# Kernel optimization log

Hardware: AMD Instinct MI355X
Metric: run time of the kernel (lower is better)

Reference implementation:

```python
import jax, jax.numpy as jnp
import numpy as np

N = 100000
E = 3200000
FIRE, WEA, TER = 8, 12, 10
H = 64


def setup_inputs() -> dict:
    key = jax.random.key(0)
    ks = jax.random.split(key, 24)
    def lin(kw, fan_in, fan_out):
        # torch nn.Linear default init: U(-1/sqrt(fan_in), 1/sqrt(fan_in))
        b = 1.0 / np.sqrt(fan_in)
        W = jax.random.uniform(kw, (fan_in, fan_out), jnp.float32, -b, b)
        return W
    inp = {
        'x_fire': jax.random.normal(ks[0], (N, FIRE), jnp.float32),
        'x_weather': jax.random.normal(ks[1], (N, WEA), jnp.float32),
        'x_terrain': jax.random.normal(ks[2], (N, TER), jnp.float32),
        'edge_index': jax.random.randint(ks[3], (2, E), 0, N, jnp.int64),
        # modality encoders
        'w_fire': lin(ks[4], FIRE, H), 'b_fire': jnp.zeros((H,), jnp.float32),
        'w_wea': lin(ks[5], WEA, H),  'b_wea': jnp.zeros((H,), jnp.float32),
        'w_ter': lin(ks[6], TER, H),  'b_ter': jnp.zeros((H,), jnp.float32),
        # GCN layers (concat fusion -> first layer in_dim = 3H)
        'gcn_w0': lin(ks[7], 3 * H, H), 'gcn_b0': jnp.zeros((H,), jnp.float32),
        'gcn_w1': lin(ks[8], H, H),     'gcn_b1': jnp.zeros((H,), jnp.float32),
        'gcn_w2': lin(ks[9], H, H),     'gcn_b2': jnp.zeros((H,), jnp.float32),
        # output MLP: H -> H//2 -> 1
        'out_w1': lin(ks[10], H, H // 2), 'out_b1': jnp.zeros((H // 2,), jnp.float32),
        'out_w2': lin(ks[11], H // 2, 1), 'out_b2': jnp.zeros((1,), jnp.float32),
    }
    return inp


def _gcn_conv(x, src, dst, W, b):
    """PyG GCNConv: h = W x; out[i] = sum_{j->i} norm_ij h[j] + self-loop + bias,
    with norm_ij = deg[i]^-1/2 * deg[j]^-1/2, deg including the added self-loop."""
    h = x @ W                                             # [N, H]
    deg = jnp.zeros((N,), h.dtype).at[dst].add(1.0) + 1.0  # +1 self-loop
    dinv = jax.lax.rsqrt(deg)                             # deg^-0.5
    norm = dinv[src] * dinv[dst]                          # [E]
    agg = jnp.zeros_like(h).at[dst].add(h[src] * norm[:, None])
    agg = agg + h * (dinv * dinv)[:, None]                # self-loop contribution
    return agg + b


def reference(x_fire, x_weather, x_terrain, edge_index,
              w_fire, b_fire, w_wea, b_wea, w_ter, b_ter,
              gcn_w0, gcn_b0, gcn_w1, gcn_b1, gcn_w2, gcn_b2,
              out_w1, out_b1, out_w2, out_b2):
    # modality encoders (eval mode: dropout is identity)
    h_fire = jax.nn.relu(x_fire @ w_fire + b_fire)
    h_wea = jax.nn.relu(x_weather @ w_wea + b_wea)
    h_ter = jax.nn.relu(x_terrain @ w_ter + b_ter)
    x = jnp.concatenate([h_fire, h_wea, h_ter], axis=1)   # [N, 3H]
    src, dst = edge_index[0], edge_index[1]
    x = jax.nn.relu(_gcn_conv(x, src, dst, gcn_w0, gcn_b0))
    x = jax.nn.relu(_gcn_conv(x, src, dst, gcn_w1, gcn_b1))
    x = jax.nn.relu(_gcn_conv(x, src, dst, gcn_w2, gcn_b2))
    out = jax.nn.relu(x @ out_w1 + out_b1) @ out_w2 + out_b2
    return out
```

## Files before the change

kernel.cpp:

```cpp
#include <hip/hip_runtime.h>

#define NN 100000
#define NE 3200000
#define HD 64

#define NBUCK 256
#define BWID 392
#define SLACK 20480
#define COLCAP 13568
#define OVFCAP 512
#define CAP 16
#define P1_EPB 2048
#define P1_GRID ((NE + P1_EPB - 1) / P1_EPB)

typedef int      v4i __attribute__((ext_vector_type(4)));
typedef int      v2i __attribute__((ext_vector_type(2)));
typedef _Float16 h4f __attribute__((ext_vector_type(4)));

__device__ __forceinline__ void fma4(float4& a, float s, const float4& b) {
    a.x = fmaf(s, b.x, a.x); a.y = fmaf(s, b.y, a.y);
    a.z = fmaf(s, b.z, a.z); a.w = fmaf(s, b.w, a.w);
}
__device__ __forceinline__ void addh4(float4& a, const h4f& b) {
    a.x += (float)b[0]; a.y += (float)b[1]; a.z += (float)b[2]; a.w += (float)b[3];
}

__global__ void __launch_bounds__(256) partition_kernel(
    const int* __restrict__ src, const int* __restrict__ dst,
    int* __restrict__ bctl, v2i* __restrict__ pairs, v2i* __restrict__ povf) {
    __shared__ v2i stage[NBUCK][CAP];
    __shared__ int cnt[NBUCK];
    int t = threadIdx.x;
    cnt[t] = 0;
    __syncthreads();
    const v4i* d4p = (const v4i*)dst;
    const v4i* s4p = (const v4i*)src;
    const int NE4 = NE / 4;
    int base4 = blockIdx.x * (P1_EPB / 4);
    #pragma unroll
    for (int it = 0; it < P1_EPB / 1024; it++) {
        int i = base4 + it * 256 + t;
        v4i d4 = (v4i){-1, -1, -1, -1};
        v4i s4 = (v4i){0, 0, 0, 0};
        if (i < NE4) {
            d4 = __builtin_nontemporal_load(d4p + i);
            s4 = __builtin_nontemporal_load(s4p + i);
        }
        #pragma unroll
        for (int k = 0; k < 4; k++) {
            int d = d4[k];
            if (d >= 0) {
                int b = (unsigned)d / BWID;
                int slot = atomicAdd(&cnt[b], 1);
                v2i p; p[0] = s4[k]; p[1] = d;
                if (slot < CAP) {
                    stage[b][slot] = p;
                } else {
                    int o = atomicAdd(&bctl[b * 16 + 2], 1);
                    if (o < OVFCAP) povf[(size_t)b * OVFCAP + o] = p;
                }
            }
        }
    }
    __syncthreads();
    int c_tot = cnt[t];
    int c = (c_tot > CAP) ? CAP : c_tot;
    int runs = (c + 7) >> 3;
    if (runs) {
        int slots = runs * 8;
        for (int m = c; m < slots; m++) { v2i p; p[0] = 0; p[1] = -1; stage[t][m] = p; }
        int gb = atomicAdd(&bctl[t * 16], slots);
        if (gb + slots <= SLACK) {
            v4i* gp = (v4i*)(pairs + (size_t)t * SLACK + gb);
            const v4i* sp = (const v4i*)&stage[t][0];
            #pragma unroll
            for (int m = 0; m < 8; m++) { if (m < runs * 4) gp[m] = sp[m]; }
        } else {
            for (int m = 0; m < slots && gb + m < SLACK; m++)
                pairs[(size_t)t * SLACK + gb + m] = stage[t][m];
        }
    }
    if (c_tot > 0) atomicAdd(&bctl[t * 16 + 1], c_tot);
}

__global__ void bucket_scan_kernel(const int* __restrict__ bctl,
                                   int* __restrict__ bbase, int* __restrict__ rowptr) {
    __shared__ int s[NBUCK];
    int t = threadIdx.x;
    int v = bctl[t * 16 + 1];
    s[t] = v; __syncthreads();
    for (int off = 1; off < NBUCK; off <<= 1) {
        int x = (t >= off) ? s[t - off] : 0;
        __syncthreads();
        s[t] += x;
        __syncthreads();
    }
    bbase[t] = s[t] - v;
    if (t == NBUCK - 1) rowptr[NN] = s[t];
}

__global__ void __launch_bounds__(256) csr_fill_kernel(
    const v2i* __restrict__ pairs, const v2i* __restrict__ povf,
    const int* __restrict__ bctl, const int* __restrict__ bbase,
    int* __restrict__ rowptr, float* __restrict__ dinv, int* __restrict__ col) {
    __shared__ int hist[BWID];
    __shared__ int rp[BWID];
    __shared__ int cur[BWID];
    __shared__ int sc[256];
    __shared__ int cols[COLCAP];
    int b = blockIdx.x, t = threadIdx.x;
    int lo = b * BWID;
    int hi = min(lo + BWID, NN);
    int nw = hi - lo;
    for (int i = t; i < BWID; i += 256) { hist[i] = 0; cur[i] = 0; }
    __syncthreads();
    int np = bctl[b * 16];     if (np > SLACK) np = SLACK;
    int nov = bctl[b * 16 + 2]; if (nov > OVFCAP) nov = OVFCAP;
    int base = bbase[b];
    const v2i* pb = pairs + (size_t)b * SLACK;
    const v2i* ob = povf + (size_t)b * OVFCAP;
    for (int i = t; i < np; i += 256) {
        v2i p = pb[i];
        if (p[1] >= 0) atomicAdd(&hist[p[1] - lo], 1);
    }
    for (int i = t; i < nov; i += 256) {
        v2i p = ob[i];
        atomicAdd(&hist[p[1] - lo], 1);
    }
    __syncthreads();
    int h0 = 0, s2 = 0;
    if (2 * t < BWID) {
        h0 = hist[2 * t];
        int h1 = (2 * t + 1 < BWID) ? hist[2 * t + 1] : 0;
        s2 = h0 + h1;
    }
    sc[t] = s2; __syncthreads();
    for (int off = 1; off < 256; off <<= 1) {
        int x = (t >= off) ? sc[t - off] : 0;
        __syncthreads();
        sc[t] += x;
        __syncthreads();
    }
    if (2 * t < BWID) {
        int ex = sc[t] - s2;
        rp[2 * t] = ex;
        if (2 * t + 1 < BWID) rp[2 * t + 1] = ex + h0;
    }
    __syncthreads();
    for (int i = t; i < nw; i += 256) {
        rowptr[lo + i] = base + rp[i];
        dinv[lo + i] = 1.0f / sqrtf((float)(hist[i] + 1));
    }
    for (int i = t; i < np; i += 256) {
        v2i p = pb[i];
        if (p[1] >= 0) {
            int li = p[1] - lo;
            int slot = atomicAdd(&cur[li], 1);
            int o = rp[li] + slot;
            if (o < COLCAP) cols[o] = p[0];
        }
    }
    for (int i = t; i < nov; i += 256) {
        v2i p = ob[i];
        int li = p[1] - lo;
        int slot = atomicAdd(&cur[li], 1);
        int o = rp[li] + slot;
        if (o < COLCAP) cols[o] = p[0];
    }
    __syncthreads();
    int nreal = bctl[b * 16 + 1]; if (nreal > COLCAP) nreal = COLCAP;
    for (int i = t; i < nreal; i += 256)
        col[base + i] = cols[i];
}

__global__ void __launch_bounds__(256) encmm0_kernel(
    const float* __restrict__ xf, const float* __restrict__ xw, const float* __restrict__ xt,
    const float* __restrict__ Wf, const float* __restrict__ bf,
    const float* __restrict__ Ww, const float* __restrict__ bw,
    const float* __restrict__ Wt, const float* __restrict__ bt,
    const float* __restrict__ W0, const float* __restrict__ dinv,
    _Float16* __restrict__ h) {
    __shared__ float xin[64][32];
    __shared__ float wenc[30][64];
    __shared__ float bs[192];
    __shared__ float xs[64][36];
    __shared__ float ws[32][64];
    int t = threadIdx.x;
    int n0 = blockIdx.x * 64;

    {
        const float4* xf4 = (const float4*)xf;
        for (int i = t; i < 128; i += 256) {
            int n = i >> 1, q = i & 1;
            int gn = n0 + n;
            float4 v = make_float4(0, 0, 0, 0);
            if (gn < NN) v = xf4[(size_t)gn * 2 + q];
            *(float4*)&xin[n][q * 4] = v;
        }
        const float4* xw4 = (const float4*)xw;
        for (int i = t; i < 192; i += 256) {
            int n = i / 3, q = i - n * 3;
            int gn = n0 + n;
            float4 v = make_float4(0, 0, 0, 0);
            if (gn < NN) v = xw4[(size_t)gn * 3 + q];
            *(float4*)&xin[n][8 + q * 4] = v;
        }
        const float2* xt2 = (const float2*)xt;
        for (int i = t; i < 320; i += 256) {
            int n = i / 5, q = i - n * 5;
            int gn = n0 + n;
            float2 v = make_float2(0, 0);
            if (gn < NN) v = xt2[(size_t)gn * 5 + q];
            *(float2*)&xin[n][20 + q * 2] = v;
        }
        for (int i = t; i < 480; i += 256) {
            int r = i >> 4, q = i & 15;
            float4 v;
            if (r < 8)       v = ((const float4*)Wf)[r * 16 + q];
            else if (r < 20) v = ((const float4*)Ww)[(r - 8) * 16 + q];
            else             v = ((const float4*)Wt)[(r - 20) * 16 + q];
            *(float4*)&wenc[r][q * 4] = v;
        }
        if (t < 192) bs[t] = (t < 64) ? bf[t] : (t < 128) ? bw[t - 64] : bt[t - 128];
    }

    int cg = t & 15, ng = t >> 4;
    int c0 = cg * 4;
    float4 acc[4];
    #pragma unroll
    for (int i = 0; i < 4; i++) acc[i] = make_float4(0, 0, 0, 0);

    for (int kq = 0; kq < 6; kq++) {
        __syncthreads();
        {
            const float4* W04 = (const float4*)W0;
            float4* ws4 = (float4*)&ws[0][0];
            for (int i = t; i < 512; i += 256)
                ws4[i] = W04[(size_t)kq * 512 + i];
        }
        int coff = (kq < 2) ? kq * 32 : (kq < 4) ? (kq - 2) * 32 : (kq - 4) * 32;
        if (kq < 2) {
            for (int i = t; i < 2048; i += 256) {
                int n = i >> 5, kk = i & 31;
                float a = bs[kq * 32 + kk];
                #pragma unroll
                for (int k = 0; k < 8; k++) a = fmaf(xin[n][k], wenc[k][coff + kk], a);
                xs[n][kk] = fmaxf(a, 0.f);
            }
        } else if (kq < 4) {
            for (int i = t; i < 2048; i += 256) {
                int n = i >> 5, kk = i & 31;
                float a = bs[kq * 32 + kk];
                #pragma unroll
                for (int k = 0; k < 12; k++) a = fmaf(xin[n][8 + k], wenc[8 + k][coff + kk], a);
                xs[n][kk] = fmaxf(a, 0.f);
            }
        } else {
            for (int i = t; i < 2048; i += 256) {
                int n = i >> 5, kk = i & 31;
                float a = bs[kq * 32 + kk];
                #pragma unroll
                for (int k = 0; k < 10; k++) a = fmaf(xin[n][20 + k], wenc[20 + k][coff + kk], a);
                xs[n][kk] = fmaxf(a, 0.f);
            }
        }
        __syncthreads();
        for (int k = 0; k < 32; k += 4) {
            float4 b0 = *(const float4*)&ws[k + 0][c0];
            float4 b1 = *(const float4*)&ws[k + 1][c0];
            float4 b2 = *(const float4*)&ws[k + 2][c0];
            float4 b3 = *(const float4*)&ws[k + 3][c0];
            #pragma unroll
            for (int i = 0; i < 4; i++) {
                float4 a = *(const float4*)&xs[ng * 4 + i][k];
                fma4(acc[i], a.x, b0); fma4(acc[i], a.y, b1);
                fma4(acc[i], a.z, b2); fma4(acc[i], a.w, b3);
            }
        }
    }
    h4f* h4 = (h4f*)h;
    #pragma unroll
    for (int i = 0; i < 4; i++) {
        int gn = n0 + ng * 4 + i;
        if (gn < NN) {
            float dn = dinv[gn];
            h4f v;
            v[0] = (_Float16)(acc[i].x * dn);
            v[1] = (_Float16)(acc[i].y * dn);
            v[2] = (_Float16)(acc[i].z * dn);
            v[3] = (_Float16)(acc[i].w * dn);
            h4[((unsigned)gn << 4) + cg] = v;
        }
    }
}

#define GATHER_BODY(E)                                              \
    {   int s_ = __shfl(pv, (E));                                   \
        h4f v_ = h4[((unsigned)s_ << 4) + q];                       \
        addh4(acc, v_); }

__global__ void gather_mm_kernel(
    const int* __restrict__ col, const int* __restrict__ rowptr,
    const float* __restrict__ dinv, const _Float16* __restrict__ h,
    const float* __restrict__ bias, const float* __restrict__ W,
    _Float16* __restrict__ hout) {
    int t = threadIdx.x;
    int n = (blockIdx.x * 256 + t) >> 6;
    int l = t & 63;
    if (n >= NN) return;
    int g = l >> 4;
    int q = l & 15;
    const h4f* h4 = (const h4f*)h;
    float dn = dinv[n];
    h4f hnh = h4[((unsigned)n << 4) + q];
    float4 b4 = ((const float4*)bias)[q];
    float4 acc = make_float4(0, 0, 0, 0);
    int r0 = rowptr[n], r1 = rowptr[n + 1];
    for (int base = r0; base < r1; base += 64) {
        int cnt = min(64, r1 - base);
        int pv = NN;
        if (l < cnt) pv = __builtin_nontemporal_load(col + base + l);
        int steps = (cnt + 3) >> 2;
        int j = 0;
        for (; j + 8 <= steps; j += 8) {
            int s0 = __shfl(pv, (j + 0) * 4 + g);
            int s1 = __shfl(pv, (j + 1) * 4 + g);
            int s2 = __shfl(pv, (j + 2) * 4 + g);
            int s3 = __shfl(pv, (j + 3) * 4 + g);
            int s4 = __shfl(pv, (j + 4) * 4 + g);
            int s5 = __shfl(pv, (j + 5) * 4 + g);
            int s6 = __shfl(pv, (j + 6) * 4 + g);
            int s7 = __shfl(pv, (j + 7) * 4 + g);
            h4f v0 = h4[((unsigned)s0 << 4) + q];
            h4f v1 = h4[((unsigned)s1 << 4) + q];
            h4f v2 = h4[((unsigned)s2 << 4) + q];
            h4f v3 = h4[((unsigned)s3 << 4) + q];
            h4f v4 = h4[((unsigned)s4 << 4) + q];
            h4f v5 = h4[((unsigned)s5 << 4) + q];
            h4f v6 = h4[((unsigned)s6 << 4) + q];
            h4f v7 = h4[((unsigned)s7 << 4) + q];
            addh4(acc, v0); addh4(acc, v1); addh4(acc, v2); addh4(acc, v3);
            addh4(acc, v4); addh4(acc, v5); addh4(acc, v6); addh4(acc, v7);
        }
        for (; j + 4 <= steps; j += 4) {
            int s0 = __shfl(pv, (j + 0) * 4 + g);
            int s1 = __shfl(pv, (j + 1) * 4 + g);
            int s2 = __shfl(pv, (j + 2) * 4 + g);
            int s3 = __shfl(pv, (j + 3) * 4 + g);
            h4f v0 = h4[((unsigned)s0 << 4) + q];
            h4f v1 = h4[((unsigned)s1 << 4) + q];
            h4f v2 = h4[((unsigned)s2 << 4) + q];
            h4f v3 = h4[((unsigned)s3 << 4) + q];
            addh4(acc, v0); addh4(acc, v1); addh4(acc, v2); addh4(acc, v3);
        }
        for (; j < steps; j++)
            GATHER_BODY(j * 4 + g)
    }
    acc.x += __shfl_xor(acc.x, 16); acc.y += __shfl_xor(acc.y, 16);
    acc.z += __shfl_xor(acc.z, 16); acc.w += __shfl_xor(acc.w, 16);
    acc.x += __shfl_xor(acc.x, 32); acc.y += __shfl_xor(acc.y, 32);
    acc.z += __shfl_xor(acc.z, 32); acc.w += __shfl_xor(acc.w, 32);
    float4 r;
    r.x = fmaxf(fmaf(dn, acc.x + (float)hnh[0], b4.x), 0.f);
    r.y = fmaxf(fmaf(dn, acc.y + (float)hnh[1], b4.y), 0.f);
    r.z = fmaxf(fmaf(dn, acc.z + (float)hnh[2], b4.z), 0.f);
    r.w = fmaxf(fmaf(dn, acc.w + (float)hnh[3], b4.w), 0.f);
    float oc0 = 0.f, oc1 = 0.f, oc2 = 0.f, oc3 = 0.f;
    #pragma unroll
    for (int qq = 0; qq < 16; qq++) {
        float rx = __shfl(r.x, qq);
        float ry = __shfl(r.y, qq);
        float rz = __shfl(r.z, qq);
        float rw = __shfl(r.w, qq);
        oc0 = fmaf(rx, W[(qq * 4 + 0) * 64 + l], oc0);
        oc1 = fmaf(ry, W[(qq * 4 + 1) * 64 + l], oc1);
        oc2 = fmaf(rz, W[(qq * 4 + 2) * 64 + l], oc2);
        oc3 = fmaf(rw, W[(qq * 4 + 3) * 64 + l], oc3);
    }
    float oc = (oc0 + oc1) + (oc2 + oc3);
    __builtin_nontemporal_store((_Float16)(oc * dn), &hout[((unsigned)n << 6) + l]);
}

__global__ void gather_mlp_kernel(
    const int* __restrict__ col, const int* __restrict__ rowptr,
    const float* __restrict__ dinv, const _Float16* __restrict__ h,
    const float* __restrict__ bias, const float* __restrict__ w1,
    const float* __restrict__ b1, const float* __restrict__ w2,
    const float* __restrict__ b2, float* __restrict__ out) {
    int t = threadIdx.x;
    int n = (blockIdx.x * 256 + t) >> 6;
    int l = t & 63;
    if (n >= NN) return;
    int g = l >> 4;
    int q = l & 15;
    const h4f* h4 = (const h4f*)h;
    float dn = dinv[n];
    h4f hnh = h4[((unsigned)n << 4) + q];
    float4 b4 = ((const float4*)bias)[q];
    float4 acc = make_float4(0, 0, 0, 0);
    int r0 = rowptr[n], r1 = rowptr[n + 1];
    for (int base = r0; base < r1; base += 64) {
        int cnt = min(64, r1 - base);
        int pv = NN;
        if (l < cnt) pv = __builtin_nontemporal_load(col + base + l);
        int steps = (cnt + 3) >> 2;
        int j = 0;
        for (; j + 8 <= steps; j += 8) {
            int s0 = __shfl(pv, (j + 0) * 4 + g);
            int s1 = __shfl(pv, (j + 1) * 4 + g);
            int s2 = __shfl(pv, (j + 2) * 4 + g);
            int s3 = __shfl(pv, (j + 3) * 4 + g);
            int s4 = __shfl(pv, (j + 4) * 4 + g);
            int s5 = __shfl(pv, (j + 5) * 4 + g);
            int s6 = __shfl(pv, (j + 6) * 4 + g);
            int s7 = __shfl(pv, (j + 7) * 4 + g);
            h4f v0 = h4[((unsigned)s0 << 4) + q];
            h4f v1 = h4[((unsigned)s1 << 4) + q];
            h4f v2 = h4[((unsigned)s2 << 4) + q];
            h4f v3 = h4[((unsigned)s3 << 4) + q];
            h4f v4 = h4[((unsigned)s4 << 4) + q];
            h4f v5 = h4[((unsigned)s5 << 4) + q];
            h4f v6 = h4[((unsigned)s6 << 4) + q];
            h4f v7 = h4[((unsigned)s7 << 4) + q];
            addh4(acc, v0); addh4(acc, v1); addh4(acc, v2); addh4(acc, v3);
            addh4(acc, v4); addh4(acc, v5); addh4(acc, v6); addh4(acc, v7);
        }
        for (; j + 4 <= steps; j += 4) {
            int s0 = __shfl(pv, (j + 0) * 4 + g);
            int s1 = __shfl(pv, (j + 1) * 4 + g);
            int s2 = __shfl(pv, (j + 2) * 4 + g);
            int s3 = __shfl(pv, (j + 3) * 4 + g);
            h4f v0 = h4[((unsigned)s0 << 4) + q];
            h4f v1 = h4[((unsigned)s1 << 4) + q];
            h4f v2 = h4[((unsigned)s2 << 4) + q];
            h4f v3 = h4[((unsigned)s3 << 4) + q];
            addh4(acc, v0); addh4(acc, v1); addh4(acc, v2); addh4(acc, v3);
        }
        for (; j < steps; j++)
            GATHER_BODY(j * 4 + g)
    }
    acc.x += __shfl_xor(acc.x, 16); acc.y += __shfl_xor(acc.y, 16);
    acc.z += __shfl_xor(acc.z, 16); acc.w += __shfl_xor(acc.w, 16);
    acc.x += __shfl_xor(acc.x, 32); acc.y += __shfl_xor(acc.y, 32);
    acc.z += __shfl_xor(acc.z, 32); acc.w += __shfl_xor(acc.w, 32);
    float4 r;
    r.x = fmaxf(fmaf(dn, acc.x + (float)hnh[0], b4.x), 0.f);
    r.y = fmaxf(fmaf(dn, acc.y + (float)hnh[1], b4.y), 0.f);
    r.z = fmaxf(fmaf(dn, acc.z + (float)hnh[2], b4.z), 0.f);
    r.w = fmaxf(fmaf(dn, acc.w + (float)hnh[3], b4.w), 0.f);
    int c = l & 31;
    float a0 = b1[c], a1 = 0.f, a2p = 0.f, a3 = 0.f;
    #pragma unroll
    for (int qq = 0; qq < 16; qq++) {
        float rx = __shfl(r.x, qq);
        float ry = __shfl(r.y, qq);
        float rz = __shfl(r.z, qq);
        float rw = __shfl(r.w, qq);
        a0  = fmaf(rx, w1[(qq * 4 + 0) * 32 + c], a0);
        a1  = fmaf(ry, w1[(qq * 4 + 1) * 32 + c], a1);
        a2p = fmaf(rz, w1[(qq * 4 + 2) * 32 + c], a2p);
        a3  = fmaf(rw, w1[(qq * 4 + 3) * 32 + c], a3);
    }
    float a = (a0 + a1) + (a2p + a3);
    float v = fmaxf(a, 0.f) * w2[c];
    v += __shfl_xor(v, 1); v += __shfl_xor(v, 2);
    v += __shfl_xor(v, 4); v += __shfl_xor(v, 8);
    v += __shfl_xor(v, 16);
    if (l == 0) __builtin_nontemporal_store(v + b2[0], &out[n]);
}

extern "C" void kernel_launch(void* const* d_in, const int* in_sizes, int n_in,
                              void* d_out, int out_size, void* d_ws, size_t ws_size,
                              hipStream_t stream) {
    const float* xf = (const float*)d_in[0];
    const float* xw = (const float*)d_in[1];
    const float* xt = (const float*)d_in[2];
    const int*   ei = (const int*)d_in[3];
    const int*   src = ei;
    const int*   dst = ei + NE;
    const float* Wf = (const float*)d_in[4];
    const float* bf = (const float*)d_in[5];
    const float* Ww = (const float*)d_in[6];
    const float* bw = (const float*)d_in[7];
    const float* Wt = (const float*)d_in[8];
    const float* bt = (const float*)d_in[9];
    const float* W0 = (const float*)d_in[10];
    const float* b0 = (const float*)d_in[11];
    const float* W1 = (const float*)d_in[12];
    const float* b1 = (const float*)d_in[13];
    const float* W2 = (const float*)d_in[14];
    const float* b2 = (const float*)d_in[15];
    const float* ow1 = (const float*)d_in[16];
    const float* ob1 = (const float*)d_in[17];
    const float* ow2 = (const float*)d_in[18];
    const float* ob2 = (const float*)d_in[19];
    float* out = (float*)d_out;

    char* w = (char*)d_ws;
    _Float16* hA  = (_Float16*)w;  w += (size_t)(NN + 1) * 64 * 2;
    _Float16* hB  = (_Float16*)w;  w += (size_t)(NN + 1) * 64 * 2;
    int*   col    = (int*)w;    w += (size_t)NE * 4;
    v2i*   pairs  = (v2i*)w;    w += (size_t)NBUCK * SLACK * 8;
    v2i*   povf   = (v2i*)w;    w += (size_t)NBUCK * OVFCAP * 8;
    float* dinv   = (float*)w;  w += (size_t)NN * 4;
    int*   rowptr = (int*)w;    w += (size_t)(NN + 1) * 4;
    int*   bctl   = (int*)w;    w += (size_t)NBUCK * 16 * 4;
    int*   bbase  = (int*)w;    w += (size_t)NBUCK * 4;

    hipMemsetAsync(bctl, 0, (size_t)NBUCK * 16 * 4, stream);
    hipMemsetAsync(hA + (size_t)NN * 64, 0, 64 * 2, stream);
    hipMemsetAsync(hB + (size_t)NN * 64, 0, 64 * 2, stream);
    partition_kernel<<<P1_GRID, 256, 0, stream>>>(src, dst, bctl, pairs, povf);
    bucket_scan_kernel<<<1, NBUCK, 0, stream>>>(bctl, bbase, rowptr);
    csr_fill_kernel<<<NBUCK, 256, 0, stream>>>(pairs, povf, bctl, bbase, rowptr, dinv, col);

    encmm0_kernel<<<(NN + 63) / 64, 256, 0, stream>>>(xf, xw, xt, Wf, bf, Ww, bw, Wt, bt, W0, dinv, hA);
    gather_mm_kernel<<<(NN * 64 + 255) / 256, 256, 0, stream>>>(col, rowptr, dinv, hA, b0, W1, hB);
    gather_mm_kernel<<<(NN * 64 + 255) / 256, 256, 0, stream>>>(col, rowptr, dinv, hB, b1, W2, hA);
    gather_mlp_kernel<<<(NN * 64 + 255) / 256, 256, 0, stream>>>(col, rowptr, dinv, hA, b2, ow1, ob1, ow2, ob2, out);
}
```

Before: 566.7 us.

## Pack edge pairs into 32-bit words and fold bucket scan into CSR fill

Each staged edge is packed into a single 32-bit word, holding the 17-bit source index plus the local destination offset shifted left by 17, instead of an 8-byte pair. This halves partition write traffic and CSR-fill read traffic. The staging capacity per bucket is raised from 16 to 24 to cut overflow spills. The separate bucket-scan kernel and two small memsets are removed: every csr_fill block now redoes the 256-entry scan itself and block 0 zeroes the padding rows, which saves launches at the cost of redundant scan work.

```diff
diff --git a/kernel.cpp b/kernel.cpp
--- a/kernel.cpp
+++ b/kernel.cpp
@@ -9,9 +9,10 @@
 #define SLACK 20480
 #define COLCAP 13568
 #define OVFCAP 512
-#define CAP 16
+#define CAP 24
 #define P1_EPB 2048
 #define P1_GRID ((NE + P1_EPB - 1) / P1_EPB)
+#define PSENT 0xFFFFFFFFu
 
 typedef int      v4i __attribute__((ext_vector_type(4)));
 typedef int      v2i __attribute__((ext_vector_type(2)));
@@ -27,8 +28,8 @@
 
 __global__ void __launch_bounds__(256) partition_kernel(
     const int* __restrict__ src, const int* __restrict__ dst,
-    int* __restrict__ bctl, v2i* __restrict__ pairs, v2i* __restrict__ povf) {
-    __shared__ v2i stage[NBUCK][CAP];
+    int* __restrict__ bctl, unsigned* __restrict__ pairs, v2i* __restrict__ povf) {
+    __shared__ unsigned stage[NBUCK][CAP];
     __shared__ int cnt[NBUCK];
     int t = threadIdx.x;
     cnt[t] = 0;
@@ -52,11 +53,12 @@
             if (d >= 0) {
                 int b = (unsigned)d / BWID;
                 int slot = atomicAdd(&cnt[b], 1);
-                v2i p; p[0] = s4[k]; p[1] = d;
+                unsigned u = (unsigned)s4[k] | ((unsigned)(d - b * BWID) << 17);
                 if (slot < CAP) {
-                    stage[b][slot] = p;
+                    stage[b][slot] = u;
                 } else {
                     int o = atomicAdd(&bctl[b * 16 + 2], 1);
+                    v2i p; p[0] = s4[k]; p[1] = d;
                     if (o < OVFCAP) povf[(size_t)b * OVFCAP + o] = p;
                 }
             }
@@ -68,13 +70,13 @@
     int runs = (c + 7) >> 3;
     if (runs) {
         int slots = runs * 8;
-        for (int m = c; m < slots; m++) { v2i p; p[0] = 0; p[1] = -1; stage[t][m] = p; }
+        for (int m = c; m < slots; m++) stage[t][m] = PSENT;
         int gb = atomicAdd(&bctl[t * 16], slots);
         if (gb + slots <= SLACK) {
             v4i* gp = (v4i*)(pairs + (size_t)t * SLACK + gb);
             const v4i* sp = (const v4i*)&stage[t][0];
             #pragma unroll
-            for (int m = 0; m < 8; m++) { if (m < runs * 4) gp[m] = sp[m]; }
+            for (int m = 0; m < 6; m++) { if (m < runs * 2) gp[m] = sp[m]; }
         } else {
             for (int m = 0; m < slots && gb + m < SLACK; m++)
                 pairs[(size_t)t * SLACK + gb + m] = stage[t][m];
@@ -83,45 +85,44 @@
     if (c_tot > 0) atomicAdd(&bctl[t * 16 + 1], c_tot);
 }
 
-__global__ void bucket_scan_kernel(const int* __restrict__ bctl,
-                                   int* __restrict__ bbase, int* __restrict__ rowptr) {
-    __shared__ int s[NBUCK];
-    int t = threadIdx.x;
-    int v = bctl[t * 16 + 1];
-    s[t] = v; __syncthreads();
-    for (int off = 1; off < NBUCK; off <<= 1) {
-        int x = (t >= off) ? s[t - off] : 0;
-        __syncthreads();
-        s[t] += x;
-        __syncthreads();
-    }
-    bbase[t] = s[t] - v;
-    if (t == NBUCK - 1) rowptr[NN] = s[t];
-}
-
 __global__ void __launch_bounds__(256) csr_fill_kernel(
-    const v2i* __restrict__ pairs, const v2i* __restrict__ povf,
-    const int* __restrict__ bctl, const int* __restrict__ bbase,
-    int* __restrict__ rowptr, float* __restrict__ dinv, int* __restrict__ col) {
+    const unsigned* __restrict__ pairs, const v2i* __restrict__ povf,
+    const int* __restrict__ bctl, int* __restrict__ rowptr,
+    float* __restrict__ dinv, int* __restrict__ col,
+    _Float16* __restrict__ hA, _Float16* __restrict__ hB) {
     __shared__ int hist[BWID];
     __shared__ int rp[BWID];
     __shared__ int cur[BWID];
     __shared__ int sc[256];
     __shared__ int cols[COLCAP];
     int b = blockIdx.x, t = threadIdx.x;
+    if (b == 0 && t < 64) {
+        hA[(size_t)NN * 64 + t] = (_Float16)0.f;
+        hB[(size_t)NN * 64 + t] = (_Float16)0.f;
+    }
     int lo = b * BWID;
     int hi = min(lo + BWID, NN);
     int nw = hi - lo;
+    int bcv = bctl[t * 16 + 1];
+    sc[t] = bcv; __syncthreads();
+    for (int off = 1; off < 256; off <<= 1) {
+        int x = (t >= off) ? sc[t - off] : 0;
+        __syncthreads();
+        sc[t] += x;
+        __syncthreads();
+    }
+    int base = (b > 0) ? sc[b - 1] : 0;
+    if (b == 0 && t == 255) rowptr[NN] = sc[255];
+    __syncthreads();
     for (int i = t; i < BWID; i += 256) { hist[i] = 0; cur[i] = 0; }
     __syncthreads();
     int np = bctl[b * 16];     if (np > SLACK) np = SLACK;
     int nov = bctl[b * 16 + 2]; if (nov > OVFCAP) nov = OVFCAP;
-    int base = bbase[b];
-    const v2i* pb = pairs + (size_t)b * SLACK;
+    const unsigned* pb = pairs + (size_t)b * SLACK;
     const v2i* ob = povf + (size_t)b * OVFCAP;
     for (int i = t; i < np; i += 256) {
-        v2i p = pb[i];
-        if (p[1] >= 0) atomicAdd(&hist[p[1] - lo], 1);
+        unsigned u = pb[i];
+        if (u != PSENT) atomicAdd(&hist[(u >> 17) & 0x1FF], 1);
     }
     for (int i = t; i < nov; i += 256) {
         v2i p = ob[i];
@@ -152,12 +153,12 @@
         dinv[lo + i] = 1.0f / sqrtf((float)(hist[i] + 1));
     }
     for (int i = t; i < np; i += 256) {
-        v2i p = pb[i];
-        if (p[1] >= 0) {
-            int li = p[1] - lo;
+        unsigned u = pb[i];
+        if (u != PSENT) {
+            int li = (u >> 17) & 0x1FF;
             int slot = atomicAdd(&cur[li], 1);
             int o = rp[li] + slot;
-            if (o < COLCAP) cols[o] = p[0];
+            if (o < COLCAP) cols[o] = (int)(u & 0x1FFFF);
         }
     }
     for (int i = t; i < nov; i += 256) {
@@ -500,19 +501,15 @@
     _Float16* hA  = (_Float16*)w;  w += (size_t)(NN + 1) * 64 * 2;
     _Float16* hB  = (_Float16*)w;  w += (size_t)(NN + 1) * 64 * 2;
     int*   col    = (int*)w;    w += (size_t)NE * 4;
-    v2i*   pairs  = (v2i*)w;    w += (size_t)NBUCK * SLACK * 8;
+    unsigned* pairs = (unsigned*)w; w += (size_t)NBUCK * SLACK * 4;
     v2i*   povf   = (v2i*)w;    w += (size_t)NBUCK * OVFCAP * 8;
     float* dinv   = (float*)w;  w += (size_t)NN * 4;
     int*   rowptr = (int*)w;    w += (size_t)(NN + 1) * 4;
     int*   bctl   = (int*)w;    w += (size_t)NBUCK * 16 * 4;
-    int*   bbase  = (int*)w;    w += (size_t)NBUCK * 4;
 
     hipMemsetAsync(bctl, 0, (size_t)NBUCK * 16 * 4, stream);
-    hipMemsetAsync(hA + (size_t)NN * 64, 0, 64 * 2, stream);
-    hipMemsetAsync(hB + (size_t)NN * 64, 0, 64 * 2, stream);
     partition_kernel<<<P1_GRID, 256, 0, stream>>>(src, dst, bctl, pairs, povf);
-    bucket_scan_kernel<<<1, NBUCK, 0, stream>>>(bctl, bbase, rowptr);
-    csr_fill_kernel<<<NBUCK, 256, 0, stream>>>(pairs, povf, bctl, bbase, rowptr, dinv, col);
+    csr_fill_kernel<<<NBUCK, 256, 0, stream>>>(pairs, povf, bctl, rowptr, dinv, col, hA, hB);
 
     encmm0_kernel<<<(NN + 63) / 64, 256, 0, stream>>>(xf, xw, xt, Wf, bf, Ww, bw, Wt, bt, W0, dinv, hA);
     gather_mm_kernel<<<(NN * 64 + 255) / 256, 256, 0, stream>>>(col, rowptr, dinv, hA, b0, W1, hB);
```

Measured after the change: 549.9 us. 1.03x faster.
